# Performance work log

Hardware: AMD Instinct MI355X
Metric: run time of the kernel (lower is better)

The kernel has to match this reference:

```python
import jax, jax.numpy as jnp
import numpy as np

N_M, N_H = 50000, 50000
E = 600000
D_IN, D_OUT = 128, 128
LN_EPS = 1e-5
NORM_EPS = 1e-12


def _segment_mean(x, seg, n):
    # PyG 'mean' aggregation: sum / count, 0 for isolated nodes (count clamped to 1)
    s = jax.ops.segment_sum(x, seg, num_segments=n)
    c = jax.ops.segment_sum(jnp.ones((seg.shape[0], 1), x.dtype), seg, num_segments=n)
    return s / jnp.maximum(c, 1.0)


def _sage(t_src, t_dst, ei, Wl, bl, Wr):
    # SAGEConv: lin_l(mean_j x_j) + lin_r(x_i), then L2-normalize rows
    agg = _segment_mean(t_src[ei[0]], ei[1], t_dst.shape[0])
    out = agg @ Wl + bl + t_dst @ Wr
    nrm = jnp.maximum(jnp.linalg.norm(out, axis=-1, keepdims=True), NORM_EPS)
    return out / nrm


def _layer_norm(x, g, b):
    mu = jnp.mean(x, axis=-1, keepdims=True)
    v = jnp.var(x, axis=-1, keepdims=True)
    return (x - mu) / jnp.sqrt(v + LN_EPS) * g + b


def setup_inputs() -> dict:
    key = jax.random.key(0)
    ks = jax.random.split(key, 24)
    r = lambda i, shape: jax.random.normal(ks[i], shape, dtype=jnp.float32) * 0.05
    inp = {
        'x_microbe': jax.random.normal(ks[0], (N_M, D_IN), dtype=jnp.float32),
        'x_host': jax.random.normal(ks[1], (N_H, D_IN), dtype=jnp.float32),
        # per-node-type linear transforms
        'W_nt_m': r(2, (D_IN, D_OUT)), 'b_nt_m': r(3, (D_OUT,)),
        'W_nt_h': r(4, (D_IN, D_OUT)), 'b_nt_h': r(5, (D_OUT,)),
        # SAGEConv params per edge type (lin_l has bias, lin_r has no bias)
        'Wl_mm': r(6, (D_OUT, D_OUT)), 'bl_mm': r(7, (D_OUT,)), 'Wr_mm': r(8, (D_OUT, D_OUT)),
        'Wl_mh': r(9, (D_OUT, D_OUT)), 'bl_mh': r(10, (D_OUT,)), 'Wr_mh': r(11, (D_OUT, D_OUT)),
        'Wl_hm': r(12, (D_OUT, D_OUT)), 'bl_hm': r(13, (D_OUT,)), 'Wr_hm': r(14, (D_OUT, D_OUT)),
        # LayerNorm affine params per node type
        'g_m': jnp.ones((D_OUT,), jnp.float32), 'be_m': jnp.zeros((D_OUT,), jnp.float32),
        'g_h': jnp.ones((D_OUT,), jnp.float32), 'be_h': jnp.zeros((D_OUT,), jnp.float32),
        # edge indices [2, E]: row0 = src, row1 = dst
        'ei_mm': jax.random.randint(ks[15], (2, E), 0, N_M, dtype=jnp.int32),
        'ei_mh': jnp.stack([jax.random.randint(ks[16], (E,), 0, N_M, dtype=jnp.int32),
                            jax.random.randint(ks[17], (E,), 0, N_H, dtype=jnp.int32)]),
        'ei_hm': jnp.stack([jax.random.randint(ks[18], (E,), 0, N_H, dtype=jnp.int32),
                            jax.random.randint(ks[19], (E,), 0, N_M, dtype=jnp.int32)]),
    }
    return inp


def reference(x_microbe, x_host, W_nt_m, b_nt_m, W_nt_h, b_nt_h,
              Wl_mm, bl_mm, Wr_mm, Wl_mh, bl_mh, Wr_mh, Wl_hm, bl_hm, Wr_hm,
              g_m, be_m, g_h, be_h, ei_mm, ei_mh, ei_hm):
    # per-type linear transforms
    t_m = x_microbe @ W_nt_m + b_nt_m
    t_h = x_host @ W_nt_h + b_nt_h
    # SAGEConv per edge type
    o_mm = _sage(t_m, t_m, ei_mm, Wl_mm, bl_mm, Wr_mm)  # microbe -> microbe
    o_mh = _sage(t_m, t_h, ei_mh, Wl_mh, bl_mh, Wr_mh)  # microbe -> host
    o_hm = _sage(t_h, t_m, ei_hm, Wl_hm, bl_hm, Wr_hm)  # host -> microbe
    # HeteroConv aggr='mean' over edge types per dst node type
    conv_m = 0.5 * (o_mm + o_hm)
    conv_h = o_mh
    # residual + LayerNorm (dropout is identity in eval mode)
    out_m = _layer_norm(t_m + conv_m, g_m, be_m)
    out_h = _layer_norm(t_h + conv_h, g_h, be_h)
    return out_m, out_h
```

## Files before the change

kernel.cpp:

```cpp
#include <hip/hip_runtime.h>

typedef unsigned short u16;
typedef unsigned int u32;
typedef __attribute__((ext_vector_type(8))) short bf16x8;
typedef __attribute__((ext_vector_type(4))) float f32x4;

__device__ __forceinline__ float bf_lo(u32 u){ return __uint_as_float(u << 16); }
__device__ __forceinline__ float bf_hi(u32 u){ return __uint_as_float(u & 0xffff0000u); }
__device__ __forceinline__ float bf2f(u16 v){ return __uint_as_float((u32)v << 16); }
__device__ __forceinline__ u16 f2bf(float f){
    u32 u = __float_as_uint(f);
    u32 r = (u + 0x7fffu + ((u >> 16) & 1u)) >> 16;
    return (u16)r;
}
__device__ __forceinline__ u32 pack2(float a, float b){
    return (u32)f2bf(a) | ((u32)f2bf(b) << 16);
}

__global__ __launch_bounds__(256) void fusedA_kernel(
    const int* __restrict__ d0, const int* __restrict__ d1, const int* __restrict__ d2,
    int* __restrict__ rk0, int* __restrict__ rk1, int* __restrict__ rk2,
    int E0, int E1, int E2, int b0, int b1, int b2, int n0, int n1, int n2,
    int* __restrict__ cnt, int h0, int h1, int h2,
    const float* __restrict__ Wf0, const float* __restrict__ Wf1,
    const float* __restrict__ Wf2, const float* __restrict__ Wf3,
    const float* __restrict__ Wf4, const float* __restrict__ Wf5,
    u16* __restrict__ WF,
    const float* __restrict__ Xm, const float* __restrict__ Wm,
    const float* __restrict__ bm, u16* __restrict__ Tm, int NM,
    const float* __restrict__ Xh, const float* __restrict__ Wh,
    const float* __restrict__ bh, u16* __restrict__ Th, int NH,
    int gm, int gh)
{
    int bid = blockIdx.x;
    int HB = h0 + h1 + h2;
    if (bid < HB){
        int t, lb;
        if (bid < h0){ t = 0; lb = bid; }
        else if (bid < h0 + h1){ t = 1; lb = bid - h0; }
        else { t = 2; lb = bid - h0 - h1; }
        const int* d = t == 0 ? d0 : (t == 1 ? d1 : d2);
        int* rk = t == 0 ? rk0 : (t == 1 ? rk1 : rk2);
        int E = t == 0 ? E0 : (t == 1 ? E1 : E2);
        int b = t == 0 ? b0 : (t == 1 ? b1 : b2);
        int n = t == 0 ? n0 : (t == 1 ? n1 : n2);
        int i = lb * 256 + threadIdx.x;
        if (i < E){
            int x = d[i];
            if ((unsigned)x < (unsigned)n) rk[i] = atomicAdd(&cnt[b + x], 1);
        }
        return;
    }
    bid -= HB;
    if (bid < 6){
        const float* W = bid == 0 ? Wf0 : bid == 1 ? Wf1 : bid == 2 ? Wf2 :
                         bid == 3 ? Wf3 : bid == 4 ? Wf4 : Wf5;
        u16* dst = WF + (size_t)bid * 16384;
        #pragma unroll 4
        for (int k = 0; k < 64; ++k){
            int i = k * 256 + threadIdx.x;
            int j   = i & 7;
            int l16 = (i >> 3) & 15;
            int qd  = (i >> 7) & 3;
            int q   = (i >> 9) & 3;
            int tt  = (i >> 11) & 1;
            int w   = (i >> 12) & 3;
            dst[i] = f2bf(W[(q * 32 + qd * 8 + j) * 128 + (w * 32 + tt * 16 + l16)]);
        }
        return;
    }
    bid -= 6;
    const float *A, *W, *bias; u16* C; int N, lgrid, lbid;
    if (bid < gm){ A = Xm; W = Wm; bias = bm; C = Tm; N = NM; lgrid = gm; lbid = bid; }
    else         { A = Xh; W = Wh; bias = bh; C = Th; N = NH; lgrid = gh; lbid = bid - gm; }

    int tid = threadIdx.x;
    int wave = tid >> 6, lane = tid & 63;
    int colHalf = wave & 1;
    int ln16 = lane & 15, quad = lane >> 4;

    bf16x8 Bfrag[4][4];
    #pragma unroll
    for (int t = 0; t < 4; ++t){
        int col = colHalf * 64 + t * 16 + ln16;
        #pragma unroll
        for (int q = 0; q < 4; ++q){
            bf16x8 f;
            #pragma unroll
            for (int j = 0; j < 8; ++j)
                f[j] = (short)f2bf(W[(q * 32 + quad * 8 + j) * 128 + col]);
            Bfrag[t][q] = f;
        }
    }
    float bv[4];
    #pragma unroll
    for (int t = 0; t < 4; ++t)
        bv[t] = bias[colHalf * 64 + t * 16 + ln16];

    int rowBlocks = (N + 15) >> 4;
    for (int rb = lbid * 2 + (wave >> 1); rb < rowBlocks; rb += lgrid * 2){
        int row0 = rb * 16;
        int ar = row0 + ln16; if (ar > N - 1) ar = N - 1;
        const float* Arow = A + (size_t)ar * 128 + quad * 8;
        bf16x8 Af[4];
        #pragma unroll
        for (int q = 0; q < 4; ++q){
            f32x4 lo = *(const f32x4*)(Arow + q * 32);
            f32x4 hi = *(const f32x4*)(Arow + q * 32 + 4);
            bf16x8 f;
            #pragma unroll
            for (int j = 0; j < 4; ++j){ f[j] = (short)f2bf(lo[j]); f[4+j] = (short)f2bf(hi[j]); }
            Af[q] = f;
        }
        f32x4 acc[4];
        #pragma unroll
        for (int t = 0; t < 4; ++t) acc[t] = (f32x4){bv[t], bv[t], bv[t], bv[t]};
        #pragma unroll
        for (int q = 0; q < 4; ++q)
            #pragma unroll
            for (int t = 0; t < 4; ++t)
                acc[t] = __builtin_amdgcn_mfma_f32_16x16x32_bf16(Af[q], Bfrag[t][q], acc[t], 0, 0, 0);
        #pragma unroll
        for (int t = 0; t < 4; ++t){
            int col = colHalf * 64 + t * 16 + ln16;
            #pragma unroll
            for (int r = 0; r < 4; ++r){
                int row = row0 + quad * 4 + r;
                if (row < N) C[(size_t)row * 128 + col] = f2bf(acc[t][r]);
            }
        }
    }
}

__global__ __launch_bounds__(256) void scan_blocks_kernel(
    const int* __restrict__ cnt, int n, int* __restrict__ off, int* __restrict__ part)
{
    __shared__ int lds[256];
    int tid = threadIdx.x;
    int base = blockIdx.x * 2048 + tid * 8;
    int v[8]; int s = 0;
    #pragma unroll
    for (int j = 0; j < 8; ++j){
        int idx = base + j;
        int c = (idx < n) ? cnt[idx] : 0;
        v[j] = s; s += c;
    }
    lds[tid] = s;
    __syncthreads();
    for (int d = 1; d < 256; d <<= 1){
        int t = (tid >= d) ? lds[tid - d] : 0;
        __syncthreads();
        lds[tid] += t;
        __syncthreads();
    }
    int thrBase = (tid > 0) ? lds[tid - 1] : 0;
    if (tid == 255) part[blockIdx.x] = lds[255];
    #pragma unroll
    for (int j = 0; j < 8; ++j){
        int idx = base + j;
        if (idx < n) off[idx] = thrBase + v[j];
    }
}

__global__ __launch_bounds__(128) void scan_part_kernel(
    int* __restrict__ part, int np, int* __restrict__ total_slot)
{
    __shared__ int lds[128];
    int tid = threadIdx.x;
    lds[tid] = (tid < np) ? part[tid] : 0;
    __syncthreads();
    for (int d = 1; d < 128; d <<= 1){
        int t = (tid >= d) ? lds[tid - d] : 0;
        __syncthreads();
        lds[tid] += t;
        __syncthreads();
    }
    if (tid < np) part[tid] = (tid > 0) ? lds[tid - 1] : 0;
    if (tid == 0) *total_slot = lds[np - 1 < 0 ? 0 : np - 1];
}

__global__ __launch_bounds__(256) void scan_add_kernel(
    int* __restrict__ off, const int* __restrict__ part, int n)
{
    int i = blockIdx.x * 256 + threadIdx.x;
    if (i < n) off[i] += part[i >> 11];
}

__global__ __launch_bounds__(256) void fill3_kernel(
    const int* __restrict__ s0, const int* __restrict__ s1, const int* __restrict__ s2,
    const int* __restrict__ d0, const int* __restrict__ d1, const int* __restrict__ d2,
    const int* __restrict__ rk0, const int* __restrict__ rk1, const int* __restrict__ rk2,
    int E0, int E1, int E2, int b0, int b1, int b2, int n0, int n1, int n2,
    const int* __restrict__ off, int* __restrict__ slot)
{
    int t = blockIdx.y;
    int i = blockIdx.x * 256 + threadIdx.x;
    const int* sp = t == 0 ? s0 : (t == 1 ? s1 : s2);
    const int* dp = t == 0 ? d0 : (t == 1 ? d1 : d2);
    const int* rk = t == 0 ? rk0 : (t == 1 ? rk1 : rk2);
    int E = t == 0 ? E0 : (t == 1 ? E1 : E2);
    int b = t == 0 ? b0 : (t == 1 ? b1 : b2);
    int n = t == 0 ? n0 : (t == 1 ? n1 : n2);
    if (i < E){
        int x = dp[i];
        if ((unsigned)x < (unsigned)n){
            slot[off[b + x] + rk[i]] = sp[i];
        }
    }
}

__global__ __launch_bounds__(256) void gather3_kernel(
    const u16* __restrict__ TM, const u16* __restrict__ TH,
    const int* __restrict__ off, const int* __restrict__ slot,
    u32* __restrict__ AGGM, u32* __restrict__ AGGH, int NM, int NH)
{
    int n3 = 2 * NM + NH;
    int wid = (int)((blockIdx.x * 256u + threadIdx.x) >> 6);
    int lane = threadIdx.x & 63;
    int nw = (gridDim.x * 256) >> 6;

    for (int id = wid; id < n3; id += nw){
        int b = off[id], e = off[id + 1];
        int deg = e - b;
        const u16* Tsrc; int nsrc;
        if (id < NM){ Tsrc = TM; nsrc = NM; }
        else if (id < 2 * NM){ Tsrc = TH; nsrc = NH; }
        else { Tsrc = TM; nsrc = NM; }

        int take = deg < 64 ? deg : 64;
        int ms = 0;
        if (lane < take){
            ms = slot[b + lane];
            if ((unsigned)ms >= (unsigned)nsrc) ms = 0;
        }

        float a0=0.f,a1=0.f,b0f=0.f,b1f=0.f,c0=0.f,c1=0.f,d0f=0.f,d1f=0.f;
        float e0=0.f,e1=0.f,f0=0.f,f1=0.f,g0=0.f,g1=0.f,h0=0.f,h1=0.f;
        int j = 0;
        for (; j + 8 <= take; j += 8){
            int i0 = __shfl(ms, j);     int i1 = __shfl(ms, j + 1);
            int i2 = __shfl(ms, j + 2); int i3 = __shfl(ms, j + 3);
            int i4 = __shfl(ms, j + 4); int i5 = __shfl(ms, j + 5);
            int i6 = __shfl(ms, j + 6); int i7 = __shfl(ms, j + 7);
            u32 u0 = *(const u32*)(Tsrc + (size_t)i0 * 128 + lane * 2);
            u32 u1 = *(const u32*)(Tsrc + (size_t)i1 * 128 + lane * 2);
            u32 u2 = *(const u32*)(Tsrc + (size_t)i2 * 128 + lane * 2);
            u32 u3 = *(const u32*)(Tsrc + (size_t)i3 * 128 + lane * 2);
            u32 u4 = *(const u32*)(Tsrc + (size_t)i4 * 128 + lane * 2);
            u32 u5 = *(const u32*)(Tsrc + (size_t)i5 * 128 + lane * 2);
            u32 u6 = *(const u32*)(Tsrc + (size_t)i6 * 128 + lane * 2);
            u32 u7 = *(const u32*)(Tsrc + (size_t)i7 * 128 + lane * 2);
            a0 += bf_lo(u0); a1 += bf_hi(u0);
            b0f += bf_lo(u1); b1f += bf_hi(u1);
            c0 += bf_lo(u2); c1 += bf_hi(u2);
            d0f += bf_lo(u3); d1f += bf_hi(u3);
            e0 += bf_lo(u4); e1 += bf_hi(u4);
            f0 += bf_lo(u5); f1 += bf_hi(u5);
            g0 += bf_lo(u6); g1 += bf_hi(u6);
            h0 += bf_lo(u7); h1 += bf_hi(u7);
        }
        for (; j + 4 <= take; j += 4){
            int i0 = __shfl(ms, j);     int i1 = __shfl(ms, j + 1);
            int i2 = __shfl(ms, j + 2); int i3 = __shfl(ms, j + 3);
            u32 u0 = *(const u32*)(Tsrc + (size_t)i0 * 128 + lane * 2);
            u32 u1 = *(const u32*)(Tsrc + (size_t)i1 * 128 + lane * 2);
            u32 u2 = *(const u32*)(Tsrc + (size_t)i2 * 128 + lane * 2);
            u32 u3 = *(const u32*)(Tsrc + (size_t)i3 * 128 + lane * 2);
            a0 += bf_lo(u0); a1 += bf_hi(u0);
            b0f += bf_lo(u1); b1f += bf_hi(u1);
            c0 += bf_lo(u2); c1 += bf_hi(u2);
            d0f += bf_lo(u3); d1f += bf_hi(u3);
        }
        for (; j < take; ++j){
            int i0 = __shfl(ms, j);
            u32 u0 = *(const u32*)(Tsrc + (size_t)i0 * 128 + lane * 2);
            a0 += bf_lo(u0); a1 += bf_hi(u0);
        }
        for (int j2 = b + 64; j2 < e; ++j2){
            int i0 = slot[j2];
            if ((unsigned)i0 >= (unsigned)nsrc) i0 = 0;
            u32 u0 = *(const u32*)(Tsrc + (size_t)i0 * 128 + lane * 2);
            a0 += bf_lo(u0); a1 += bf_hi(u0);
        }
        float s0 = ((a0 + b0f) + (c0 + d0f)) + ((e0 + f0) + (g0 + h0));
        float s1 = ((a1 + b1f) + (c1 + d1f)) + ((e1 + f1) + (g1 + h1));
        float inv = 1.0f / (float)(deg < 1 ? 1 : deg);
        u32 pv = pack2(s0 * inv, s1 * inv);
        if (id < 2 * NM) AGGM[(size_t)id * 64 + lane] = pv;
        else             AGGH[(size_t)(id - 2 * NM) * 64 + lane] = pv;
    }
}

template<int NT>
__global__ __launch_bounds__(256) void gemmln_kernel(
    const u32* __restrict__ AG1, const u32* __restrict__ AG2,
    const u16* __restrict__ Tdst,
    const u16* __restrict__ WFl1, const u16* __restrict__ WFr1, const float* __restrict__ bl1,
    const u16* __restrict__ WFl2, const u16* __restrict__ WFr2, const float* __restrict__ bl2,
    const float* __restrict__ g, const float* __restrict__ be,
    float* __restrict__ outp, int N, float scale)
{
    __shared__ float redN[NT][4][16];
    __shared__ float redS[2][4][16];

    int tid = threadIdx.x;
    int wave = tid >> 6, lane = tid & 63;
    int ln16 = lane & 15, quad = lane >> 4;

    const u32* AG[2] = {AG1, AG2};
    const u16* WFl[2] = {WFl1, WFl2};
    const u16* WFr[2] = {WFr1, WFr2};
    const float* bls[2] = {bl1, bl2};

    bf16x8 BL[NT][2][4], BR[NT][2][4];
    float bv[NT][2];
    #pragma unroll
    for (int et = 0; et < NT; ++et){
        #pragma unroll
        for (int t = 0; t < 2; ++t){
            bv[et][t] = bls[et][wave * 32 + t * 16 + ln16];
            #pragma unroll
            for (int q = 0; q < 4; ++q){
                int fo = ((((wave * 2 + t) * 4 + q) * 4 + quad) * 16 + ln16) * 8;
                BL[et][t][q] = *(const bf16x8*)(WFl[et] + fo);
                BR[et][t][q] = *(const bf16x8*)(WFr[et] + fo);
            }
        }
    }
    float gv[2], bev[2];
    #pragma unroll
    for (int t = 0; t < 2; ++t){
        int col = wave * 32 + t * 16 + ln16;
        gv[t] = g[col]; bev[t] = be[col];
    }

    int tiles = (N + 15) >> 4;
    for (int tile = blockIdx.x; tile < tiles; tile += gridDim.x){
        int row0 = tile * 16;
        int ar = row0 + ln16; if (ar > N - 1) ar = N - 1;
        const u16* Ar2 = Tdst + (size_t)ar * 128 + quad * 8;

        f32x4 acc[NT][2];
        #pragma unroll
        for (int et = 0; et < NT; ++et)
            #pragma unroll
            for (int t = 0; t < 2; ++t)
                acc[et][t] = (f32x4){bv[et][t], bv[et][t], bv[et][t], bv[et][t]};

        #pragma unroll
        for (int q = 0; q < 4; ++q){
            bf16x8 afr = *(const bf16x8*)(Ar2 + q * 32);
            #pragma unroll
            for (int et = 0; et < NT; ++et){
                bf16x8 afl = *(const bf16x8*)(AG[et] + (size_t)ar * 64 + q * 16 + quad * 4);
                #pragma unroll
                for (int t = 0; t < 2; ++t){
                    acc[et][t] = __builtin_amdgcn_mfma_f32_16x16x32_bf16(afl, BL[et][t][q], acc[et][t], 0, 0, 0);
                    acc[et][t] = __builtin_amdgcn_mfma_f32_16x16x32_bf16(afr, BR[et][t][q], acc[et][t], 0, 0, 0);
                }
            }
        }

        #pragma unroll
        for (int et = 0; et < NT; ++et){
            #pragma unroll
            for (int r = 0; r < 4; ++r){
                float s = acc[et][0][r] * acc[et][0][r] + acc[et][1][r] * acc[et][1][r];
                #pragma unroll
                for (int m = 1; m < 16; m <<= 1) s += __shfl_xor(s, m);
                if (ln16 == 0) redN[et][wave][quad * 4 + r] = s;
            }
        }
        __syncthreads();

        float yv[2][4];
        float lsum[4], lsq[4];
        #pragma unroll
        for (int r = 0; r < 4; ++r){
            int r16 = quad * 4 + r;
            int row = row0 + r16;
            int crow = row < N ? row : N - 1;
            float sc[NT];
            #pragma unroll
            for (int et = 0; et < NT; ++et){
                float tot = redN[et][0][r16] + redN[et][1][r16] + redN[et][2][r16] + redN[et][3][r16];
                sc[et] = scale / fmaxf(sqrtf(tot), 1e-12f);
            }
            float s1v = 0.f, s2v = 0.f;
            #pragma unroll
            for (int t = 0; t < 2; ++t){
                int col = wave * 32 + t * 16 + ln16;
                float y = bf2f(Tdst[(size_t)crow * 128 + col]);
                #pragma unroll
                for (int et = 0; et < NT; ++et) y += acc[et][t][r] * sc[et];
                yv[t][r] = y;
                s1v += y; s2v += y * y;
            }
            #pragma unroll
            for (int m = 1; m < 16; m <<= 1){ s1v += __shfl_xor(s1v, m); s2v += __shfl_xor(s2v, m); }
            lsum[r] = s1v; lsq[r] = s2v;
        }
        if (ln16 == 0){
            #pragma unroll
            for (int r = 0; r < 4; ++r){
                redS[0][wave][quad * 4 + r] = lsum[r];
                redS[1][wave][quad * 4 + r] = lsq[r];
            }
        }
        __syncthreads();

        #pragma unroll
        for (int r = 0; r < 4; ++r){
            int r16 = quad * 4 + r;
            int row = row0 + r16;
            if (row >= N) continue;
            float S1 = redS[0][0][r16] + redS[0][1][r16] + redS[0][2][r16] + redS[0][3][r16];
            float S2 = redS[1][0][r16] + redS[1][1][r16] + redS[1][2][r16] + redS[1][3][r16];
            float mean = S1 * (1.0f / 128.0f);
            float var = S2 * (1.0f / 128.0f) - mean * mean;
            float rstd = rsqrtf(var + 1e-5f);
            #pragma unroll
            for (int t = 0; t < 2; ++t){
                int col = wave * 32 + t * 16 + ln16;
                outp[(size_t)row * 128 + col] = (yv[t][r] - mean) * rstd * gv[t] + bev[t];
            }
        }
        __syncthreads();
    }
}

extern "C" void kernel_launch(void* const* d_in, const int* in_sizes, int n_in,
                              void* d_out, int out_size, void* d_ws, size_t ws_size,
                              hipStream_t stream) {
    const float* xm    = (const float*)d_in[0];
    const float* xh    = (const float*)d_in[1];
    const float* Wnt_m = (const float*)d_in[2];  const float* bnt_m = (const float*)d_in[3];
    const float* Wnt_h = (const float*)d_in[4];  const float* bnt_h = (const float*)d_in[5];
    const float* Wl_mm = (const float*)d_in[6];  const float* bl_mm = (const float*)d_in[7];
    const float* Wr_mm = (const float*)d_in[8];
    const float* Wl_mh = (const float*)d_in[9];  const float* bl_mh = (const float*)d_in[10];
    const float* Wr_mh = (const float*)d_in[11];
    const float* Wl_hm = (const float*)d_in[12]; const float* bl_hm = (const float*)d_in[13];
    const float* Wr_hm = (const float*)d_in[14];
    const float* g_m   = (const float*)d_in[15]; const float* be_m  = (const float*)d_in[16];
    const float* g_h   = (const float*)d_in[17]; const float* be_h  = (const float*)d_in[18];
    const int* ei_mm = (const int*)d_in[19];
    const int* ei_mh = (const int*)d_in[20];
    const int* ei_hm = (const int*)d_in[21];

    const int D = 128;
    const int NM = in_sizes[0] / D;
    const int NH = in_sizes[1] / D;
    const int E1 = in_sizes[19] / 2;
    const int E2 = in_sizes[20] / 2;
    const int E3 = in_sizes[21] / 2;
    const int Esum = E1 + E2 + E3;
    const int n3 = 2 * NM + NH;

    char* ws = (char*)d_ws;
    size_t woff = 0;
    auto alloc = [&](size_t bytes) -> void* {
        void* p = ws + woff;
        woff += (bytes + 255) & ~(size_t)255;
        return p;
    };
    u16* T_M   = (u16*)alloc((size_t)NM * D * 2);
    u16* T_H   = (u16*)alloc((size_t)NH * D * 2);
    int* CNT3  = (int*)alloc((size_t)n3 * 4);
    int* OFF3  = (int*)alloc((size_t)(n3 + 1) * 4);
    int* SLOT3 = (int*)alloc((size_t)Esum * 4);
    int* PART  = (int*)alloc(1024 * 4);
    u16* WF    = (u16*)alloc((size_t)6 * 16384 * 2);
    u32* AGGM  = (u32*)alloc((size_t)2 * NM * 64 * 4);
    if (woff > ws_size) return;

    int* RANK3 = (int*)d_out;
    int* rk0 = RANK3, *rk1 = RANK3 + E1, *rk2 = RANK3 + E1 + E3;
    u32* AGGH = (u32*)d_out;

    float* OUT_M = (float*)d_out;
    float* OUT_H = (float*)d_out + (size_t)NM * D;

    const int b0 = 0, b1 = NM, b2 = 2 * NM;
    const int h0 = (E1 + 255) / 256, h1 = (E3 + 255) / 256, h2 = (E2 + 255) / 256;
    const int gm = 1024, gh = 1024;
    int Emax = E1 > E2 ? E1 : E2; if (E3 > Emax) Emax = E3;
    const dim3 egrid((Emax + 255) / 256, 3);
    const int scanBlocks = (n3 + 2047) / 2048;

    hipMemsetAsync(CNT3, 0, (size_t)n3 * 4, stream);

    fusedA_kernel<<<h0 + h1 + h2 + 6 + gm + gh, 256, 0, stream>>>(
        ei_mm + E1, ei_hm + E3, ei_mh + E2,
        rk0, rk1, rk2,
        E1, E3, E2, b0, b1, b2, NM, NM, NH, CNT3, h0, h1, h2,
        Wl_mm, Wr_mm, Wl_hm, Wr_hm, Wl_mh, Wr_mh, WF,
        xm, Wnt_m, bnt_m, T_M, NM,
        xh, Wnt_h, bnt_h, T_H, NH, gm, gh);

    scan_blocks_kernel<<<scanBlocks, 256, 0, stream>>>(CNT3, n3, OFF3, PART);
    scan_part_kernel<<<1, 128, 0, stream>>>(PART, scanBlocks, OFF3 + n3);
    scan_add_kernel<<<(n3 + 255) / 256, 256, 0, stream>>>(OFF3, PART, n3);
    fill3_kernel<<<egrid, 256, 0, stream>>>(
        ei_mm, ei_hm, ei_mh,
        ei_mm + E1, ei_hm + E3, ei_mh + E2,
        rk0, rk1, rk2,
        E1, E3, E2, b0, b1, b2, NM, NM, NH, OFF3, SLOT3);

    gather3_kernel<<<2048, 256, 0, stream>>>(
        T_M, T_H, OFF3, SLOT3, AGGM, AGGH, NM, NH);

    gemmln_kernel<1><<<1024, 256, 0, stream>>>(
        AGGH, nullptr, T_H,
        WF + 4 * 16384, WF + 5 * 16384, bl_mh,
        nullptr, nullptr, nullptr,
        g_h, be_h, OUT_H, NH, 1.0f);
    gemmln_kernel<2><<<1024, 256, 0, stream>>>(
        AGGM, AGGM + (size_t)NM * 64, T_M,
        WF + 0 * 16384, WF + 1 * 16384, bl_mm,
        WF + 2 * 16384, WF + 3 * 16384, bl_hm,
        g_m, be_m, OUT_M, NM, 0.5f);
}
```

Before: 442.4 us.

## Privatize degree-count atomics into eight partitioned counter planes

Measured after the change: 470.7 us. 6.4% more time.

```diff
diff --git a/kernel.cpp b/kernel.cpp
--- a/kernel.cpp
+++ b/kernel.cpp
@@ -21,7 +21,7 @@
     const int* __restrict__ d0, const int* __restrict__ d1, const int* __restrict__ d2,
     int* __restrict__ rk0, int* __restrict__ rk1, int* __restrict__ rk2,
     int E0, int E1, int E2, int b0, int b1, int b2, int n0, int n1, int n2,
-    int* __restrict__ cnt, int h0, int h1, int h2,
+    int* __restrict__ cnt8, int n3s, int h0, int h1, int h2,
     const float* __restrict__ Wf0, const float* __restrict__ Wf1,
     const float* __restrict__ Wf2, const float* __restrict__ Wf3,
     const float* __restrict__ Wf4, const float* __restrict__ Wf5,
@@ -44,10 +44,17 @@
         int E = t == 0 ? E0 : (t == 1 ? E1 : E2);
         int b = t == 0 ? b0 : (t == 1 ? b1 : b2);
         int n = t == 0 ? n0 : (t == 1 ? n1 : n2);
-        int i = lb * 256 + threadIdx.x;
-        if (i < E){
-            int x = d[i];
-            if ((unsigned)x < (unsigned)n) rk[i] = atomicAdd(&cnt[b + x], 1);
+        int pl = bid & 7;
+        int* cp = cnt8 + (size_t)pl * n3s + b;
+        int base = lb * 1024 + threadIdx.x;
+        #pragma unroll
+        for (int k = 0; k < 4; ++k){
+            int i = base + k * 256;
+            if (i < E){
+                int x = d[i];
+                if ((unsigned)x < (unsigned)n)
+                    rk[i] = atomicAdd(&cp[x], 1) | (pl << 24);
+            }
         }
         return;
     }
@@ -133,7 +140,8 @@
 }
 
 __global__ __launch_bounds__(256) void scan_blocks_kernel(
-    const int* __restrict__ cnt, int n, int* __restrict__ off, int* __restrict__ part)
+    const int* __restrict__ cnt8, int n, int n3s,
+    int* __restrict__ off, int* __restrict__ base8, int* __restrict__ part)
 {
     __shared__ int lds[256];
     int tid = threadIdx.x;
@@ -142,8 +150,12 @@
     #pragma unroll
     for (int j = 0; j < 8; ++j){
         int idx = base + j;
-        int c = (idx < n) ? cnt[idx] : 0;
-        v[j] = s; s += c;
+        int tot = 0;
+        if (idx < n){
+            #pragma unroll
+            for (int x = 0; x < 8; ++x) tot += cnt8[(size_t)x * n3s + idx];
+        }
+        v[j] = s; s += tot;
     }
     lds[tid] = s;
     __syncthreads();
@@ -158,7 +170,15 @@
     #pragma unroll
     for (int j = 0; j < 8; ++j){
         int idx = base + j;
-        if (idx < n) off[idx] = thrBase + v[j];
+        if (idx < n){
+            int run = thrBase + v[j];
+            off[idx] = run;
+            #pragma unroll
+            for (int x = 0; x < 8; ++x){
+                base8[(size_t)x * n3s + idx] = run;
+                run += cnt8[(size_t)x * n3s + idx];
+            }
+        }
     }
 }
 
@@ -180,10 +200,16 @@
 }
 
 __global__ __launch_bounds__(256) void scan_add_kernel(
-    int* __restrict__ off, const int* __restrict__ part, int n)
+    int* __restrict__ off, int* __restrict__ base8, int n3s,
+    const int* __restrict__ part, int n)
 {
     int i = blockIdx.x * 256 + threadIdx.x;
-    if (i < n) off[i] += part[i >> 11];
+    if (i < n){
+        int p = part[i >> 11];
+        off[i] += p;
+        #pragma unroll
+        for (int x = 0; x < 8; ++x) base8[(size_t)x * n3s + i] += p;
+    }
 }
 
 __global__ __launch_bounds__(256) void fill3_kernel(
@@ -191,20 +217,26 @@
     const int* __restrict__ d0, const int* __restrict__ d1, const int* __restrict__ d2,
     const int* __restrict__ rk0, const int* __restrict__ rk1, const int* __restrict__ rk2,
     int E0, int E1, int E2, int b0, int b1, int b2, int n0, int n1, int n2,
-    const int* __restrict__ off, int* __restrict__ slot)
+    const int* __restrict__ base8, int n3s, int* __restrict__ slot)
 {
     int t = blockIdx.y;
-    int i = blockIdx.x * 256 + threadIdx.x;
     const int* sp = t == 0 ? s0 : (t == 1 ? s1 : s2);
     const int* dp = t == 0 ? d0 : (t == 1 ? d1 : d2);
     const int* rk = t == 0 ? rk0 : (t == 1 ? rk1 : rk2);
     int E = t == 0 ? E0 : (t == 1 ? E1 : E2);
     int b = t == 0 ? b0 : (t == 1 ? b1 : b2);
     int n = t == 0 ? n0 : (t == 1 ? n1 : n2);
-    if (i < E){
-        int x = dp[i];
-        if ((unsigned)x < (unsigned)n){
-            slot[off[b + x] + rk[i]] = sp[i];
+    int base = blockIdx.x * 1024 + threadIdx.x;
+    #pragma unroll
+    for (int k = 0; k < 4; ++k){
+        int i = base + k * 256;
+        if (i < E){
+            int x = dp[i];
+            if ((unsigned)x < (unsigned)n){
+                int r = rk[i];
+                int pl = (r >> 24) & 7;
+                slot[base8[(size_t)pl * n3s + b + x] + (r & 0xffffff)] = sp[i];
+            }
         }
     }
 }
@@ -466,7 +498,8 @@
     };
     u16* T_M   = (u16*)alloc((size_t)NM * D * 2);
     u16* T_H   = (u16*)alloc((size_t)NH * D * 2);
-    int* CNT3  = (int*)alloc((size_t)n3 * 4);
+    int* CNT8  = (int*)alloc((size_t)8 * n3 * 4);
+    int* BASE8 = (int*)alloc((size_t)8 * n3 * 4);
     int* OFF3  = (int*)alloc((size_t)(n3 + 1) * 4);
     int* SLOT3 = (int*)alloc((size_t)Esum * 4);
     int* PART  = (int*)alloc(1024 * 4);
@@ -482,30 +515,30 @@
     float* OUT_H = (float*)d_out + (size_t)NM * D;
 
     const int b0 = 0, b1 = NM, b2 = 2 * NM;
-    const int h0 = (E1 + 255) / 256, h1 = (E3 + 255) / 256, h2 = (E2 + 255) / 256;
+    const int h0 = (E1 + 1023) / 1024, h1 = (E3 + 1023) / 1024, h2 = (E2 + 1023) / 1024;
     const int gm = 1024, gh = 1024;
     int Emax = E1 > E2 ? E1 : E2; if (E3 > Emax) Emax = E3;
-    const dim3 egrid((Emax + 255) / 256, 3);
+    const dim3 egrid((Emax + 1023) / 1024, 3);
     const int scanBlocks = (n3 + 2047) / 2048;
 
-    hipMemsetAsync(CNT3, 0, (size_t)n3 * 4, stream);
+    hipMemsetAsync(CNT8, 0, (size_t)8 * n3 * 4, stream);
 
     fusedA_kernel<<<h0 + h1 + h2 + 6 + gm + gh, 256, 0, stream>>>(
         ei_mm + E1, ei_hm + E3, ei_mh + E2,
         rk0, rk1, rk2,
-        E1, E3, E2, b0, b1, b2, NM, NM, NH, CNT3, h0, h1, h2,
+        E1, E3, E2, b0, b1, b2, NM, NM, NH, CNT8, n3, h0, h1, h2,
         Wl_mm, Wr_mm, Wl_hm, Wr_hm, Wl_mh, Wr_mh, WF,
         xm, Wnt_m, bnt_m, T_M, NM,
         xh, Wnt_h, bnt_h, T_H, NH, gm, gh);
 
-    scan_blocks_kernel<<<scanBlocks, 256, 0, stream>>>(CNT3, n3, OFF3, PART);
+    scan_blocks_kernel<<<scanBlocks, 256, 0, stream>>>(CNT8, n3, n3, OFF3, BASE8, PART);
     scan_part_kernel<<<1, 128, 0, stream>>>(PART, scanBlocks, OFF3 + n3);
-    scan_add_kernel<<<(n3 + 255) / 256, 256, 0, stream>>>(OFF3, PART, n3);
+    scan_add_kernel<<<(n3 + 255) / 256, 256, 0, stream>>>(OFF3, BASE8, n3, PART, n3);
     fill3_kernel<<<egrid, 256, 0, stream>>>(
         ei_mm, ei_hm, ei_mh,
         ei_mm + E1, ei_hm + E3, ei_mh + E2,
         rk0, rk1, rk2,
-        E1, E3, E2, b0, b1, b2, NM, NM, NH, OFF3, SLOT3);
+        E1, E3, E2, b0, b1, b2, NM, NM, NH, BASE8, n3, SLOT3);
 
     gather3_kernel<<<2048, 256, 0, stream>>>(
         T_M, T_H, OFF3, SLOT3, AGGM, AGGH, NM, NH);
```

## Replace global atomic CSR build with LDS-privatized chunked histograms

Applied to the files above, without the earlier changes.

Result: slower. 476.6 us (+7.7%).

```diff
diff --git a/kernel.cpp b/kernel.cpp
--- a/kernel.cpp
+++ b/kernel.cpp
@@ -4,6 +4,9 @@
 typedef unsigned int u32;
 typedef __attribute__((ext_vector_type(8))) short bf16x8;
 typedef __attribute__((ext_vector_type(4))) float f32x4;
+
+#define LDSN 13312
+#define CHUNK 24576
 
 __device__ __forceinline__ float bf_lo(u32 u){ return __uint_as_float(u << 16); }
 __device__ __forceinline__ float bf_hi(u32 u){ return __uint_as_float(u & 0xffff0000u); }
@@ -17,11 +20,11 @@
     return (u32)f2bf(a) | ((u32)f2bf(b) << 16);
 }
 
-__global__ __launch_bounds__(256) void fusedA_kernel(
+__global__ __launch_bounds__(256) void prep_kernel(
     const int* __restrict__ d0, const int* __restrict__ d1, const int* __restrict__ d2,
-    int* __restrict__ rk0, int* __restrict__ rk1, int* __restrict__ rk2,
-    int E0, int E1, int E2, int b0, int b1, int b2, int n0, int n1, int n2,
-    int* __restrict__ cnt, int h0, int h1, int h2,
+    int E0, int E1, int E2, int n0, int n1, int n2,
+    int c0, int c1, int c2, int R0, int R1, int R2,
+    u16* __restrict__ C0, u16* __restrict__ C1, u16* __restrict__ C2, int HB2,
     const float* __restrict__ Wf0, const float* __restrict__ Wf1,
     const float* __restrict__ Wf2, const float* __restrict__ Wf3,
     const float* __restrict__ Wf4, const float* __restrict__ Wf5,
@@ -32,26 +35,28 @@
     const float* __restrict__ bh, u16* __restrict__ Th, int NH,
     int gm, int gh)
 {
+    __shared__ u32 lc[LDSN];
     int bid = blockIdx.x;
-    int HB = h0 + h1 + h2;
-    if (bid < HB){
-        int t, lb;
-        if (bid < h0){ t = 0; lb = bid; }
-        else if (bid < h0 + h1){ t = 1; lb = bid - h0; }
-        else { t = 2; lb = bid - h0 - h1; }
-        const int* d = t == 0 ? d0 : (t == 1 ? d1 : d2);
-        int* rk = t == 0 ? rk0 : (t == 1 ? rk1 : rk2);
-        int E = t == 0 ? E0 : (t == 1 ? E1 : E2);
-        int b = t == 0 ? b0 : (t == 1 ? b1 : b2);
-        int n = t == 0 ? n0 : (t == 1 ? n1 : n2);
-        int i = lb * 256 + threadIdx.x;
-        if (i < E){
-            int x = d[i];
-            if ((unsigned)x < (unsigned)n) rk[i] = atomicAdd(&cnt[b + x], 1);
-        }
+    if (bid < HB2){
+        const int* dp; int E, n, cc, rr; u16* cp;
+        if (bid < c0 * R0){ dp = d0; E = E0; n = n0; cp = C0; cc = bid / R0; rr = bid % R0; }
+        else if (bid < c0 * R0 + c1 * R1){ int l = bid - c0 * R0; dp = d1; E = E1; n = n1; cp = C1; cc = l / R1; rr = l % R1; }
+        else { int l = bid - c0 * R0 - c1 * R1; dp = d2; E = E2; n = n2; cp = C2; cc = l / R2; rr = l % R2; }
+        for (int i = threadIdx.x; i < LDSN; i += 256) lc[i] = 0;
+        __syncthreads();
+        int r0 = rr * LDSN, r1 = min(r0 + LDSN, n);
+        int i0 = cc * CHUNK, i1 = min(i0 + CHUNK, E);
+        for (int i = i0 + threadIdx.x; i < i1; i += 256){
+            int x = dp[i];
+            if ((unsigned)x < (unsigned)n && x >= r0 && x < r1)
+                atomicAdd(&lc[x - r0], 1u);
+        }
+        __syncthreads();
+        u16* op = cp + (size_t)cc * n;
+        for (int x = r0 + threadIdx.x; x < r1; x += 256) op[x] = (u16)lc[x - r0];
         return;
     }
-    bid -= HB;
+    bid -= HB2;
     if (bid < 6){
         const float* W = bid == 0 ? Wf0 : bid == 1 ? Wf1 : bid == 2 ? Wf2 :
                          bid == 3 ? Wf3 : bid == 4 ? Wf4 : Wf5;
@@ -133,7 +138,9 @@
 }
 
 __global__ __launch_bounds__(256) void scan_blocks_kernel(
-    const int* __restrict__ cnt, int n, int* __restrict__ off, int* __restrict__ part)
+    const u16* __restrict__ C0, const u16* __restrict__ C1, const u16* __restrict__ C2,
+    int c0, int c1, int c2, int NM, int NH, int n,
+    int* __restrict__ off, int* __restrict__ part)
 {
     __shared__ int lds[256];
     int tid = threadIdx.x;
@@ -142,8 +149,15 @@
     #pragma unroll
     for (int j = 0; j < 8; ++j){
         int idx = base + j;
-        int c = (idx < n) ? cnt[idx] : 0;
-        v[j] = s; s += c;
+        int tot = 0;
+        if (idx < n){
+            const u16* cp; int ch, w, x;
+            if (idx < NM){ cp = C0; ch = c0; w = NM; x = idx; }
+            else if (idx < 2 * NM){ cp = C1; ch = c1; w = NM; x = idx - NM; }
+            else { cp = C2; ch = c2; w = NH; x = idx - 2 * NM; }
+            for (int cc = 0; cc < ch; ++cc) tot += cp[(size_t)cc * w + x];
+        }
+        v[j] = s; s += tot;
     }
     lds[tid] = s;
     __syncthreads();
@@ -186,25 +200,49 @@
     if (i < n) off[i] += part[i >> 11];
 }
 
-__global__ __launch_bounds__(256) void fill3_kernel(
+__global__ __launch_bounds__(256) void colbase_kernel(
+    const u16* __restrict__ C0, const u16* __restrict__ C1, const u16* __restrict__ C2,
+    int* __restrict__ B0, int* __restrict__ B1, int* __restrict__ B2,
+    int c0, int c1, int c2, int NM, int NH, int n,
+    const int* __restrict__ off)
+{
+    int idx = blockIdx.x * 256 + threadIdx.x;
+    if (idx >= n) return;
+    const u16* cp; int* bp; int ch, w, x;
+    if (idx < NM){ cp = C0; bp = B0; ch = c0; w = NM; x = idx; }
+    else if (idx < 2 * NM){ cp = C1; bp = B1; ch = c1; w = NM; x = idx - NM; }
+    else { cp = C2; bp = B2; ch = c2; w = NH; x = idx - 2 * NM; }
+    int run = off[idx];
+    for (int cc = 0; cc < ch; ++cc){
+        bp[(size_t)cc * w + x] = run;
+        run += cp[(size_t)cc * w + x];
+    }
+}
+
+__global__ __launch_bounds__(256) void fillL_kernel(
     const int* __restrict__ s0, const int* __restrict__ s1, const int* __restrict__ s2,
     const int* __restrict__ d0, const int* __restrict__ d1, const int* __restrict__ d2,
-    const int* __restrict__ rk0, const int* __restrict__ rk1, const int* __restrict__ rk2,
-    int E0, int E1, int E2, int b0, int b1, int b2, int n0, int n1, int n2,
-    const int* __restrict__ off, int* __restrict__ slot)
-{
-    int t = blockIdx.y;
-    int i = blockIdx.x * 256 + threadIdx.x;
-    const int* sp = t == 0 ? s0 : (t == 1 ? s1 : s2);
-    const int* dp = t == 0 ? d0 : (t == 1 ? d1 : d2);
-    const int* rk = t == 0 ? rk0 : (t == 1 ? rk1 : rk2);
-    int E = t == 0 ? E0 : (t == 1 ? E1 : E2);
-    int b = t == 0 ? b0 : (t == 1 ? b1 : b2);
-    int n = t == 0 ? n0 : (t == 1 ? n1 : n2);
-    if (i < E){
+    int E0, int E1, int E2, int n0, int n1, int n2,
+    int c0, int c1, int c2, int R0, int R1, int R2,
+    const int* __restrict__ B0, const int* __restrict__ B1, const int* __restrict__ B2,
+    int* __restrict__ slot)
+{
+    __shared__ u32 lc[LDSN];
+    int bid = blockIdx.x;
+    const int *dp, *sp, *bp; int E, n, cc, rr;
+    if (bid < c0 * R0){ sp = s0; dp = d0; E = E0; n = n0; bp = B0; cc = bid / R0; rr = bid % R0; }
+    else if (bid < c0 * R0 + c1 * R1){ int l = bid - c0 * R0; sp = s1; dp = d1; E = E1; n = n1; bp = B1; cc = l / R1; rr = l % R1; }
+    else { int l = bid - c0 * R0 - c1 * R1; sp = s2; dp = d2; E = E2; n = n2; bp = B2; cc = l / R2; rr = l % R2; }
+    for (int i = threadIdx.x; i < LDSN; i += 256) lc[i] = 0;
+    __syncthreads();
+    int r0 = rr * LDSN, r1 = min(r0 + LDSN, n);
+    const int* bpc = bp + (size_t)cc * n;
+    int i0 = cc * CHUNK, i1 = min(i0 + CHUNK, E);
+    for (int i = i0 + threadIdx.x; i < i1; i += 256){
         int x = dp[i];
-        if ((unsigned)x < (unsigned)n){
-            slot[off[b + x] + rk[i]] = sp[i];
+        if ((unsigned)x < (unsigned)n && x >= r0 && x < r1){
+            u32 lr = atomicAdd(&lc[x - r0], 1u);
+            slot[bpc[x] + (int)lr] = sp[i];
         }
     }
 }
@@ -457,6 +495,14 @@
     const int Esum = E1 + E2 + E3;
     const int n3 = 2 * NM + NH;
 
+    const int c0 = (E1 + CHUNK - 1) / CHUNK;
+    const int c1 = (E3 + CHUNK - 1) / CHUNK;
+    const int c2 = (E2 + CHUNK - 1) / CHUNK;
+    const int R0 = (NM + LDSN - 1) / LDSN;
+    const int R1 = (NM + LDSN - 1) / LDSN;
+    const int R2 = (NH + LDSN - 1) / LDSN;
+    const int HB2 = c0 * R0 + c1 * R1 + c2 * R2;
+
     char* ws = (char*)d_ws;
     size_t woff = 0;
     auto alloc = [&](size_t bytes) -> void* {
@@ -466,7 +512,7 @@
     };
     u16* T_M   = (u16*)alloc((size_t)NM * D * 2);
     u16* T_H   = (u16*)alloc((size_t)NH * D * 2);
-    int* CNT3  = (int*)alloc((size_t)n3 * 4);
+    u16* CNT16 = (u16*)alloc(((size_t)(c0 + c1) * NM + (size_t)c2 * NH) * 2);
     int* OFF3  = (int*)alloc((size_t)(n3 + 1) * 4);
     int* SLOT3 = (int*)alloc((size_t)Esum * 4);
     int* PART  = (int*)alloc(1024 * 4);
@@ -474,38 +520,43 @@
     u32* AGGM  = (u32*)alloc((size_t)2 * NM * 64 * 4);
     if (woff > ws_size) return;
 
-    int* RANK3 = (int*)d_out;
-    int* rk0 = RANK3, *rk1 = RANK3 + E1, *rk2 = RANK3 + E1 + E3;
+    u16* C0p = CNT16;
+    u16* C1p = C0p + (size_t)c0 * NM;
+    u16* C2p = C1p + (size_t)c1 * NM;
+
+    int* B0p = (int*)d_out;
+    int* B1p = B0p + (size_t)c0 * NM;
+    int* B2p = B1p + (size_t)c1 * NM;
     u32* AGGH = (u32*)d_out;
 
     float* OUT_M = (float*)d_out;
     float* OUT_H = (float*)d_out + (size_t)NM * D;
 
-    const int b0 = 0, b1 = NM, b2 = 2 * NM;
-    const int h0 = (E1 + 255) / 256, h1 = (E3 + 255) / 256, h2 = (E2 + 255) / 256;
     const int gm = 1024, gh = 1024;
-    int Emax = E1 > E2 ? E1 : E2; if (E3 > Emax) Emax = E3;
-    const dim3 egrid((Emax + 255) / 256, 3);
     const int scanBlocks = (n3 + 2047) / 2048;
 
-    hipMemsetAsync(CNT3, 0, (size_t)n3 * 4, stream);
-
-    fusedA_kernel<<<h0 + h1 + h2 + 6 + gm + gh, 256, 0, stream>>>(
+    prep_kernel<<<HB2 + 6 + gm + gh, 256, 0, stream>>>(
         ei_mm + E1, ei_hm + E3, ei_mh + E2,
-        rk0, rk1, rk2,
-        E1, E3, E2, b0, b1, b2, NM, NM, NH, CNT3, h0, h1, h2,
+        E1, E3, E2, NM, NM, NH,
+        c0, c1, c2, R0, R1, R2,
+        C0p, C1p, C2p, HB2,
         Wl_mm, Wr_mm, Wl_hm, Wr_hm, Wl_mh, Wr_mh, WF,
         xm, Wnt_m, bnt_m, T_M, NM,
         xh, Wnt_h, bnt_h, T_H, NH, gm, gh);
 
-    scan_blocks_kernel<<<scanBlocks, 256, 0, stream>>>(CNT3, n3, OFF3, PART);
+    scan_blocks_kernel<<<scanBlocks, 256, 0, stream>>>(
+        C0p, C1p, C2p, c0, c1, c2, NM, NH, n3, OFF3, PART);
     scan_part_kernel<<<1, 128, 0, stream>>>(PART, scanBlocks, OFF3 + n3);
     scan_add_kernel<<<(n3 + 255) / 256, 256, 0, stream>>>(OFF3, PART, n3);
-    fill3_kernel<<<egrid, 256, 0, stream>>>(
+    colbase_kernel<<<(n3 + 255) / 256, 256, 0, stream>>>(
+        C0p, C1p, C2p, B0p, B1p, B2p, c0, c1, c2, NM, NH, n3, OFF3);
+
+    fillL_kernel<<<HB2, 256, 0, stream>>>(
         ei_mm, ei_hm, ei_mh,
         ei_mm + E1, ei_hm + E3, ei_mh + E2,
-        rk0, rk1, rk2,
-        E1, E3, E2, b0, b1, b2, NM, NM, NH, OFF3, SLOT3);
+        E1, E3, E2, NM, NM, NH,
+        c0, c1, c2, R0, R1, R2,
+        B0p, B1p, B2p, SLOT3);
 
     gather3_kernel<<<2048, 256, 0, stream>>>(
         T_M, T_H, OFF3, SLOT3, AGGM, AGGH, NM, NH);
```
